# Kernel optimization log

Hardware: AMD Instinct MI355X
Metric: run time of the kernel (lower is better)

## Reference

```python
import jax, jax.numpy as jnp
import numpy as np

EPS = 1e-12
W_MAX = 0.8
ALPHA_MAX = 1.5
T = 10
ETA = 0.2
ALPHA_SCALE = 1.0
N = 50000
IN_DIM = 512
HID = 256
C = 8
EH = 64
E2 = 400000  # undirected pairs; E = 2*E2 directed edges


def setup_inputs() -> dict:
    key = jax.random.key(0)
    ks = jax.random.split(key, 12)
    x = jax.random.normal(ks[0], (N, IN_DIM), jnp.float32)
    src0 = jax.random.randint(ks[1], (E2,), 0, N)
    dst0 = jax.random.randint(ks[2], (E2,), 0, N)
    edge_index = jnp.concatenate([jnp.stack([src0, dst0]), jnp.stack([dst0, src0])], axis=1)
    rev = jnp.concatenate([jnp.arange(E2) + E2, jnp.arange(E2)])
    def lin(k, i, o):
        return jax.random.normal(k, (i, o), jnp.float32) * (2.0 / i) ** 0.5
    enc_w1 = lin(ks[3], IN_DIM, HID); enc_b1 = jnp.zeros((HID,), jnp.float32)
    enc_w2 = lin(ks[4], HID, C); enc_b2 = jnp.zeros((C,), jnp.float32)
    edge_w1 = lin(ks[5], 2 * HID + 2, EH); edge_b1 = jnp.zeros((EH,), jnp.float32)
    edge_w2 = lin(ks[6], EH, 1); edge_b2 = jnp.zeros((1,), jnp.float32)
    bound = (6.0 / (C + C)) ** 0.5  # xavier_uniform
    R_raw = jax.random.uniform(ks[7], (C, C), jnp.float32, -bound, bound) + 0.5 * jnp.eye(C, dtype=jnp.float32)
    R_scale_log = jnp.float32(0.0)
    msg_logit = jnp.float32(-3.0)
    return dict(x=x, edge_index=edge_index, rev=rev,
                enc_w1=enc_w1, enc_b1=enc_b1, enc_w2=enc_w2, enc_b2=enc_b2,
                edge_w1=edge_w1, edge_b1=edge_b1, edge_w2=edge_w2, edge_b2=edge_b2,
                R_raw=R_raw, R_scale_log=R_scale_log, msg_logit=msg_logit)


def reference(x, edge_index, rev, enc_w1, enc_b1, enc_w2, enc_b2,
              edge_w1, edge_b1, edge_w2, edge_b2, R_raw, R_scale_log, msg_logit):
    num_nodes = x.shape[0]
    src, dst = edge_index[0], edge_index[1]
    # unary encoder (mlp type, eval mode -> no dropout)
    h = jax.nn.relu(x @ enc_w1 + enc_b1)
    logits = h @ enc_w2 + enc_b2
    log_phi = jax.nn.log_softmax(logits, axis=-1)  # [N, C]
    # structural edge features from out-degree of src
    deg = jax.ops.segment_sum(jnp.ones_like(src, jnp.float32), src, num_segments=num_nodes)
    logdeg = jnp.log(deg + 1.0)
    a, b = logdeg[src], logdeg[dst]
    struct = jnp.stack([a + b, jnp.abs(a - b)], axis=-1)  # [E, 2]
    # learned symmetric edge weights -> per-edge kernel K
    hs, hd = h[src], h[dst]
    edge_in = jnp.concatenate([hs * hd, jnp.abs(hs - hd), struct], axis=-1)  # [E, 2H+2]
    eh = jax.nn.relu(edge_in @ edge_w1 + edge_b1)
    w_raw = (eh @ edge_w2 + edge_b2)[:, 0]
    w = W_MAX * jax.nn.sigmoid(w_raw)
    w = 0.5 * (w + w[rev])
    R = 0.5 * (R_raw + R_raw.T)
    R = (jax.nn.softplus(R_scale_log) + 1e-06) * jnp.tanh(R)
    K = jnp.exp(w[:, None, None] * R[None])  # [E, C, C]
    degc = jnp.maximum(deg, 1.0)
    edge_norm = (degc[src] * degc[dst]) ** -0.5  # [E]
    alpha = ALPHA_MAX * jax.nn.sigmoid(msg_logit) * ALPHA_SCALE
    lp_src = log_phi[src]
    m = jax.nn.softmax(lp_src, axis=-1)  # init_unary=True

    def step(m, _):
        f = jnp.einsum('ec,ecd->ed', m, K)
        log_f = jnp.log(jnp.maximum(f, EPS)) * edge_norm[:, None]
        sum_in = jax.ops.segment_sum(log_f, dst, num_segments=num_nodes)
        excl = sum_in[src] - log_f[rev]
        m_new = jax.nn.softmax(lp_src + alpha * excl, axis=-1)
        m = (1.0 - ETA) * m + ETA * m_new
        m = jnp.maximum(m, EPS)
        m = m / m.sum(axis=-1, keepdims=True)
        return m, None

    m, _ = jax.lax.scan(step, m, None, length=T)
    # beliefs
    f = jnp.einsum('ec,ecd->ed', m, K)
    log_f = jnp.log(jnp.maximum(f, EPS)) * edge_norm[:, None]
    sum_in = jax.ops.segment_sum(log_f, dst, num_segments=num_nodes)
    beliefs = jax.nn.softmax(log_phi + alpha * sum_in, axis=-1)
    return beliefs
```

## Files before the change

kernel.cpp:

```cpp
#include <hip/hip_runtime.h>
#include <cstddef>
#include <cstdint>

typedef _Float16 h4 __attribute__((ext_vector_type(4)));
typedef _Float16 h8 __attribute__((ext_vector_type(8)));
typedef float    f4 __attribute__((ext_vector_type(4)));
typedef int      i4 __attribute__((ext_vector_type(4)));

#define NN      50000
#define IND     512
#define HIDN    256
#define E2P     400000
#define EDD     800000
#define NBLK    196
#define SCN     50176
#define EBLK    1563
#define DBLK    3125

#define OFF_HF16    ((size_t)0)
#define OFF_LOGF    ((size_t)0)
#define OFF_Z       ((size_t)25600000)
#define OFF_DEG     ((size_t)28800000)
#define OFF_LOGDEG  ((size_t)29004800)
#define OFF_DEGC    ((size_t)29204800)
#define OFF_BASE    ((size_t)29404800)
#define OFF_CNT     ((size_t)29609600)
#define OFF_BLK     ((size_t)29814400)
#define OFF_WT      ((size_t)29818496)
#define OFF_BT      ((size_t)30080640)
#define OFF_RS      ((size_t)30150272)
#define OFF_WSYM    ((size_t)30150784)
#define OFF_POS     ((size_t)31750784)
#define OFF_ORDER   ((size_t)34950784)
#define OFF_BASE2   ((size_t)36550784)
#define OFF_OFS2    ((size_t)36755584)
#define OFF_EIS     ((size_t)36960384)
#define OFF_M2      ((size_t)40160384)
#define OFF_REC     ((size_t)52960384)
#define WS_NEED     ((size_t)65760384)

__device__ __forceinline__ int key2(int s, int d) {
    return ((s >> 10) << 10) | (d >> 6);
}

__device__ __forceinline__ int xcd_swz(int bid, int nwg) {
    int q = nwg >> 3, r = nwg & 7;
    int x = bid & 7, idx = bid >> 3;
    return (x < r ? x * (q + 1) : r * (q + 1) + (x - r) * q) + idx;
}

__global__ void k_deg(const int* __restrict__ ei, int* __restrict__ deg,
                      int* __restrict__ cnt2) {
    int e = blockIdx.x * 256 + threadIdx.x;
    int v = ei[e];
    atomicAdd(&deg[v], 1);
    if (e < E2P) {
        int d = ei[EDD + e];
        atomicAdd(&cnt2[key2(v, d)], 1);
    }
}

__global__ void k_node(const int* __restrict__ deg, float* __restrict__ logdeg,
                       float* __restrict__ degc) {
    int n = blockIdx.x * 256 + threadIdx.x;
    if (n < NN) {
        float d = (float)deg[n];
        logdeg[n] = logf(d + 1.0f);
        degc[n]   = fmaxf(d, 1.0f);
    }
}

__global__ void k_scan1(const int* __restrict__ deg, int* __restrict__ incl,
                        int* __restrict__ blk) {
    __shared__ int sm[256];
    int i = blockIdx.x * 256 + threadIdx.x;
    int v = deg[i];
    sm[threadIdx.x] = v;
    __syncthreads();
    for (int off = 1; off < 256; off <<= 1) {
        int t = (threadIdx.x >= off) ? sm[threadIdx.x - off] : 0;
        __syncthreads();
        sm[threadIdx.x] += t;
        __syncthreads();
    }
    incl[i] = sm[threadIdx.x];
    if (threadIdx.x == 255) blk[blockIdx.x] = sm[255];
}

__global__ void k_scan2(int* __restrict__ blk) {
    __shared__ int sm[256];
    int v = (threadIdx.x < NBLK) ? blk[threadIdx.x] : 0;
    sm[threadIdx.x] = v;
    __syncthreads();
    for (int off = 1; off < 256; off <<= 1) {
        int t = (threadIdx.x >= off) ? sm[threadIdx.x - off] : 0;
        __syncthreads();
        sm[threadIdx.x] += t;
        __syncthreads();
    }
    if (threadIdx.x < NBLK) blk[threadIdx.x] = sm[threadIdx.x];
}

__global__ void k_scan3(const int* __restrict__ incl, const int* __restrict__ deg,
                        const int* __restrict__ blk, int* __restrict__ base) {
    int i = blockIdx.x * 256 + threadIdx.x;
    int off = (blockIdx.x > 0) ? blk[blockIdx.x - 1] : 0;
    base[i] = off + incl[i] - deg[i];
}

__global__ void k_pos(const int* __restrict__ ei, const int* __restrict__ base,
                      int* __restrict__ cnt, int* __restrict__ pos) {
    int e = blockIdx.x * 256 + threadIdx.x;
    int dstn = ei[EDD + e];
    pos[e] = base[dstn] + atomicAdd(&cnt[dstn], 1);
}

__global__ void k_order(const int* __restrict__ ei, const int* __restrict__ base2,
                        int* __restrict__ ofs2, int* __restrict__ order) {
    int p = blockIdx.x * 256 + threadIdx.x;
    if (p < E2P) {
        int k = key2(ei[p], ei[EDD + p]);
        order[base2[k] + atomicAdd(&ofs2[k], 1)] = p;
    }
}

__global__ void k_gath(const int* __restrict__ ei, const int* __restrict__ order,
                       int2* __restrict__ eiS) {
    int i = blockIdx.x * 256 + threadIdx.x;
    if (i < E2P) {
        int p = order[i];
        eiS[i] = make_int2(ei[p], ei[EDD + p]);
    }
}

__global__ void k_prep(const float* __restrict__ enc_w1, const float* __restrict__ edge_w1,
                       const float* __restrict__ R_raw, const float* __restrict__ Rsl,
                       const float* __restrict__ mlog,
                       _Float16* __restrict__ Wt, _Float16* __restrict__ Bt,
                       float* __restrict__ Rs) {
    int gid = blockIdx.x * 256 + threadIdx.x;
    if (gid < 256 * 512) {
        int n = gid >> 9, k = gid & 511;
        Wt[n * 512 + k] = (_Float16)enc_w1[k * 256 + n];
        return;
    }
    int g2 = gid - 256 * 512;
    if (g2 < 64 * 544) {
        int n = g2 / 544, k = g2 - n * 544;
        float v = 0.0f;
        if (k < 512) {
            int tm = k >> 5, r = k & 31;
            int qq = r >> 3, jj = (r >> 1) & 3, typ = k & 1;
            int c = (tm >> 1) * 32 + qq * 8 + (tm & 1) * 4 + jj;
            v = edge_w1[(typ ? 256 + c : c) * 64 + n];
        } else if (k < 514) {
            v = edge_w1[k * 64 + n];
        }
        Bt[n * 544 + k] = (_Float16)v;
        return;
    }
    int g3 = g2 - 64 * 544;
    if (g3 < 64) {
        int c = g3 >> 3, d = g3 & 7;
        float rv = 0.5f * (R_raw[c * 8 + d] + R_raw[d * 8 + c]);
        float s  = log1pf(expf(Rsl[0])) + 1e-6f;
        Rs[g3] = s * tanhf(rv);
        return;
    }
    if (g3 == 64) {
        Rs[64] = 1.5f / (1.0f + expf(-mlog[0]));
    }
}

__global__ __launch_bounds__(256) void k_enc(const float* __restrict__ x,
                                             const _Float16* __restrict__ Wt,
                                             const float* __restrict__ b1,
                                             _Float16* __restrict__ hf) {
    __shared__ _Float16 WL[2][256 * 40];
    const int tid = threadIdx.x;
    const int wid = tid >> 6;
    const int lane = tid & 63;
    const int l15 = lane & 15;
    const int q = lane >> 4;
    const int m0 = blockIdx.x * 64;
    const int row = m0 + wid * 16 + l15;
    const bool ract = (row < NN);
    const float* xrow = x + (size_t)row * IND;

    f4 acc[16];
#pragma unroll
    for (int i = 0; i < 16; i++) acc[i] = (f4){0.f, 0.f, 0.f, 0.f};

    const int wn  = tid >> 2;
    const int wo  = (tid & 3) * 8;

    h8 wreg[4];
#pragma unroll
    for (int rep = 0; rep < 4; rep++)
        wreg[rep] = *(const h8*)(Wt + (size_t)(rep * 64 + wn) * IND + wo);
    f4 xa = (f4){0, 0, 0, 0}, xb = (f4){0, 0, 0, 0};
    if (ract) {
        const f4* xp = (const f4*)(xrow + q * 8);
        xa = xp[0]; xb = xp[1];
    }

    for (int kt = 0; kt < 16; kt++) {
        const int cur = kt & 1;
#pragma unroll
        for (int rep = 0; rep < 4; rep++)
            *(h8*)&WL[cur][(rep * 64 + wn) * 40 + wo] = wreg[rep];
        __syncthreads();
        f4 xa2, xb2;
        if (kt < 15) {
            const int kc = (kt + 1) * 32;
#pragma unroll
            for (int rep = 0; rep < 4; rep++)
                wreg[rep] = *(const h8*)(Wt + (size_t)(rep * 64 + wn) * IND + kc + wo);
            if (ract) {
                const f4* xp = (const f4*)(xrow + kc + q * 8);
                xa2 = xp[0]; xb2 = xp[1];
            }
        }
        h8 a;
#pragma unroll
        for (int u = 0; u < 4; u++) { a[u] = (_Float16)xa[u]; a[4 + u] = (_Float16)xb[u]; }
#pragma unroll
        for (int nt = 0; nt < 16; nt++) {
            h8 b = *(const h8*)&WL[cur][(nt * 16 + l15) * 40 + q * 8];
            acc[nt] = __builtin_amdgcn_mfma_f32_16x16x32_f16(a, b, acc[nt], 0, 0, 0);
        }
        if (kt < 15 && ract) { xa = xa2; xb = xb2; }
        __syncthreads();
    }
#pragma unroll
    for (int nt = 0; nt < 16; nt++) {
        int col = nt * 16 + l15;
        float bv = b1[col];
#pragma unroll
        for (int reg = 0; reg < 4; reg++) {
            int orow = m0 + wid * 16 + q * 4 + reg;
            if (orow < NN) {
                float v = acc[nt][reg] + bv;
                hf[(size_t)orow * HIDN + col] = (_Float16)fmaxf(v, 0.f);
            }
        }
    }
}

__global__ void k_logits(const _Float16* __restrict__ hf, const float* __restrict__ w2,
                         const float* __restrict__ b2, float* __restrict__ Z) {
    __shared__ float w2L[2048];
    for (int i = threadIdx.x; i < 2048; i += 256) w2L[i] = w2[i];
    __syncthreads();
    int n = blockIdx.x * 256 + threadIdx.x;
    if (n >= NN) return;
    float sum[8];
#pragma unroll
    for (int c = 0; c < 8; c++) sum[c] = b2[c];
    for (int kb = 0; kb < 32; kb++) {
        h8 hv = *(const h8*)(hf + (size_t)n * HIDN + kb * 8);
#pragma unroll
        for (int u = 0; u < 8; u++) {
            float hx = (float)hv[u];
            const float* wr = &w2L[(kb * 8 + u) * 8];
#pragma unroll
            for (int c = 0; c < 8; c++) sum[c] += hx * wr[c];
        }
    }
    float mx = sum[0];
#pragma unroll
    for (int c = 1; c < 8; c++) mx = fmaxf(mx, sum[c]);
    float se = 0.f;
#pragma unroll
    for (int c = 0; c < 8; c++) se += __expf(sum[c] - mx);
    float lse = __logf(se);
#pragma unroll
    for (int c = 0; c < 8; c++) Z[(size_t)n * 16 + c] = sum[c] - mx - lse;
}

__global__ __launch_bounds__(256) void k_edge(const int2* __restrict__ eiS,
        const _Float16* __restrict__ hf, const float* __restrict__ logdeg,
        const _Float16* __restrict__ BtG, const float* __restrict__ eb1,
        const float* __restrict__ ew2, const float* __restrict__ eb2,
        float* __restrict__ wsym2) {
    __shared__ _Float16 BtL[64 * 136];
    const int tid = threadIdx.x;
    const int wid = tid >> 6;
    const int lane = tid & 63;
    const int l15 = lane & 15;
    const int q = lane >> 4;
    const int eb = xcd_swz(blockIdx.x, gridDim.x) * 128;

    int sidx[2], didx[2];
    float la[2], lb[2];
#pragma unroll
    for (int mt = 0; mt < 2; mt++) {
        int e = eb + wid * 32 + mt * 16 + l15;
        int2 sd = eiS[e];
        sidx[mt] = sd.x;
        didx[mt] = sd.y;
        la[mt] = logdeg[sidx[mt]];
        lb[mt] = logdeg[didx[mt]];
    }

    f4 acc[2][4];
#pragma unroll
    for (int a = 0; a < 2; a++)
#pragma unroll
        for (int b = 0; b < 4; b++) acc[a][b] = (f4){0.f, 0.f, 0.f, 0.f};

    const _Float16* hq = hf + q * 8;
    h8 curS[2], curD[2];
#pragma unroll
    for (int mt = 0; mt < 2; mt++) {
        curS[mt] = *(const h8*)(hq + (size_t)sidx[mt] * HIDN);
        curD[mt] = *(const h8*)(hq + (size_t)didx[mt] * HIDN);
    }

    for (int ph = 0; ph < 4; ph++) {
        __syncthreads();
        {
            const int r = tid >> 2;
            const int c0 = tid & 3;
            const int kbase = ph * 128;
#pragma unroll
            for (int i2 = 0; i2 < 4; i2++) {
                int ck = c0 + i2 * 4;
                *(h8*)&BtL[r * 136 + ck * 8] =
                    *(const h8*)(BtG + (size_t)r * 544 + kbase + ck * 8);
            }
        }
        __syncthreads();
#pragma unroll
        for (int kk2 = 0; kk2 < 2; kk2++) {
            const int kk = ph * 2 + kk2;
            h8 nxtS[2], nxtD[2];
            if (kk < 7) {
                const int c1 = (kk + 1) * 32;
#pragma unroll
                for (int mt = 0; mt < 2; mt++) {
                    nxtS[mt] = *(const h8*)(hq + (size_t)sidx[mt] * HIDN + c1);
                    nxtD[mt] = *(const h8*)(hq + (size_t)didx[mt] * HIDN + c1);
                }
            }
            const int ko = kk2 * 64 + q * 8;
            {
                h8 a0[2];
#pragma unroll
                for (int mt = 0; mt < 2; mt++) {
#pragma unroll
                    for (int j = 0; j < 4; j++) {
                        float x1 = (float)curS[mt][j], x2 = (float)curD[mt][j];
                        a0[mt][2 * j]     = (_Float16)(x1 * x2);
                        a0[mt][2 * j + 1] = (_Float16)fabsf(x1 - x2);
                    }
                }
                h8 bf[4];
#pragma unroll
                for (int nt = 0; nt < 4; nt++)
                    bf[nt] = *(const h8*)&BtL[(nt * 16 + l15) * 136 + ko];
#pragma unroll
                for (int mt = 0; mt < 2; mt++)
#pragma unroll
                    for (int nt = 0; nt < 4; nt++)
                        acc[mt][nt] = __builtin_amdgcn_mfma_f32_16x16x32_f16(a0[mt], bf[nt], acc[mt][nt], 0, 0, 0);
            }
            {
                h8 a1[2];
#pragma unroll
                for (int mt = 0; mt < 2; mt++) {
#pragma unroll
                    for (int j = 0; j < 4; j++) {
                        float x1 = (float)curS[mt][4 + j], x2 = (float)curD[mt][4 + j];
                        a1[mt][2 * j]     = (_Float16)(x1 * x2);
                        a1[mt][2 * j + 1] = (_Float16)fabsf(x1 - x2);
                    }
                }
                h8 bf[4];
#pragma unroll
                for (int nt = 0; nt < 4; nt++)
                    bf[nt] = *(const h8*)&BtL[(nt * 16 + l15) * 136 + ko + 32];
#pragma unroll
                for (int mt = 0; mt < 2; mt++)
#pragma unroll
                    for (int nt = 0; nt < 4; nt++)
                        acc[mt][nt] = __builtin_amdgcn_mfma_f32_16x16x32_f16(a1[mt], bf[nt], acc[mt][nt], 0, 0, 0);
            }
            if (kk < 7) {
#pragma unroll
                for (int mt = 0; mt < 2; mt++) { curS[mt] = nxtS[mt]; curD[mt] = nxtD[mt]; }
            }
        }
    }

    __syncthreads();
    {
        const int r = tid >> 2, ck = tid & 3;
        *(h8*)&BtL[r * 136 + ck * 8] = *(const h8*)(BtG + (size_t)r * 544 + 512 + ck * 8);
    }
    __syncthreads();
    {
        h8 bf[4];
#pragma unroll
        for (int nt = 0; nt < 4; nt++)
            bf[nt] = *(const h8*)&BtL[(nt * 16 + l15) * 136 + q * 8];
#pragma unroll
        for (int mt = 0; mt < 2; mt++) {
            h8 a = (h8){0, 0, 0, 0, 0, 0, 0, 0};
            if (q == 0) {
                a[0] = (_Float16)(la[mt] + lb[mt]);
                a[1] = (_Float16)fabsf(la[mt] - lb[mt]);
            }
#pragma unroll
            for (int nt = 0; nt < 4; nt++)
                acc[mt][nt] = __builtin_amdgcn_mfma_f32_16x16x32_f16(a, bf[nt], acc[mt][nt], 0, 0, 0);
        }
    }

    float b1v[4], w2v[4];
#pragma unroll
    for (int nt = 0; nt < 4; nt++) {
        int col = nt * 16 + l15;
        b1v[nt] = eb1[col];
        w2v[nt] = ew2[col];
    }
    const float b2s = eb2[0];
    float part[2][4];
#pragma unroll
    for (int mt = 0; mt < 2; mt++)
#pragma unroll
        for (int reg = 0; reg < 4; reg++) {
            float s = 0.f;
#pragma unroll
            for (int nt = 0; nt < 4; nt++) {
                float v = acc[mt][nt][reg] + b1v[nt];
                s += fmaxf(v, 0.f) * w2v[nt];
            }
            part[mt][reg] = s;
        }
#pragma unroll
    for (int off = 1; off < 16; off <<= 1)
#pragma unroll
        for (int mt = 0; mt < 2; mt++)
#pragma unroll
            for (int reg = 0; reg < 4; reg++)
                part[mt][reg] += __shfl_xor(part[mt][reg], off, 64);
    if (l15 == 0) {
#pragma unroll
        for (int mt = 0; mt < 2; mt++)
#pragma unroll
            for (int reg = 0; reg < 4; reg++) {
                int er = eb + wid * 32 + mt * 16 + q * 4 + reg;
                if (er < E2P) {
                    float xr = part[mt][reg] + b2s;
                    wsym2[er] = 0.8f / (1.0f + __expf(-xr));
                }
            }
    }
}


__device__ __forceinline__ void kprod1(const float* __restrict__ RsL, float w,
                                       const float* m, float* f) {
#pragma unroll
    for (int d = 0; d < 8; d++) f[d] = 0.f;
#pragma unroll
    for (int c = 0; c < 8; c++) {
        {
            float kv = __expf(w * RsL[c * 8 + c]);
            f[c] += m[c] * kv;
        }
#pragma unroll
        for (int d = c + 1; d < 8; d++) {
            float kv = __expf(w * RsL[c * 8 + d]);
            f[d] += m[c] * kv;
            f[c] += m[d] * kv;
        }
    }
}

__global__ __launch_bounds__(256) void k_init(const int2* __restrict__ eiS,
        const float* __restrict__ wsym2, const float* __restrict__ degc,
        const float* __restrict__ Rs, const float* __restrict__ Z,
        const int* __restrict__ pos, const int* __restrict__ order,
        i4* __restrict__ rec, _Float16* __restrict__ M2,
        _Float16* __restrict__ logf) {
    __shared__ float RsL[64];
    const int tid = threadIdx.x;
    if (tid < 64) RsL[tid] = Rs[tid];
    __syncthreads();
    int i = xcd_swz(blockIdx.x, EBLK) * 256 + tid;
    if (i >= E2P) return;
    int p = order[i];
    int2 sd = eiS[i];
    int sp = sd.x, dp = sd.y;
    float w = wsym2[i];
    float nrm = rsqrtf(degc[sp] * degc[dp]);
    int pz0 = pos[p], pz1 = pos[E2P + p];
    rec[2 * i]     = (i4){sp, pz0, (int)__float_as_int(w), (int)__float_as_int(nrm)};
    rec[2 * i + 1] = (i4){dp, pz1, (int)__float_as_int(w), (int)__float_as_int(nrm)};
    const f4* Zs = (const f4*)(Z + (size_t)sp * 16);
    const f4* Zd = (const f4*)(Z + (size_t)dp * 16);
    f4 ls0 = Zs[0], ls1 = Zs[1], ld0 = Zd[0], ld1 = Zd[1];
    float lps[8], lpd[8];
#pragma unroll
    for (int u = 0; u < 4; u++) { lps[u] = ls0[u]; lps[4+u] = ls1[u]; lpd[u] = ld0[u]; lpd[4+u] = ld1[u]; }
    float me[8], mr[8];
    {
        float mx = lps[0], mx2 = lpd[0];
#pragma unroll
        for (int d = 1; d < 8; d++) { mx = fmaxf(mx, lps[d]); mx2 = fmaxf(mx2, lpd[d]); }
        float s = 0.f, s2 = 0.f;
#pragma unroll
        for (int d = 0; d < 8; d++) { me[d] = __expf(lps[d] - mx); s += me[d];
                                      mr[d] = __expf(lpd[d] - mx2); s2 += mr[d]; }
        float rs = 1.f / s, rs2 = 1.f / s2;
#pragma unroll
        for (int d = 0; d < 8; d++) { me[d] *= rs; mr[d] *= rs2; }
    }
    {
        h8 mh, mh2;
#pragma unroll
        for (int d = 0; d < 8; d++) { mh[d] = (_Float16)me[d]; mh2[d] = (_Float16)mr[d]; }
        *(h8*)(M2 + (size_t)(2 * i) * 8)     = mh;
        *(h8*)(M2 + (size_t)(2 * i + 1) * 8) = mh2;
    }
    float fe[8], fr[8];
    kprod1(RsL, w, me, fe);
    kprod1(RsL, w, mr, fr);
    h8 le, lr;
#pragma unroll
    for (int d = 0; d < 8; d++) {
        le[d] = (_Float16)(__logf(fmaxf(fe[d], 1e-12f)) * nrm);
        lr[d] = (_Float16)(__logf(fmaxf(fr[d], 1e-12f)) * nrm);
    }
    *(h8*)(logf + (size_t)pz0 * 8) = le;
    *(h8*)(logf + (size_t)pz1 * 8) = lr;
}

__global__ __launch_bounds__(256) void k_bp2(const i4* __restrict__ rec,
        const float* __restrict__ Rs, const float* __restrict__ Z,
        _Float16* __restrict__ M2, _Float16* __restrict__ logf) {
    __shared__ float RsL[64];
    const int tid = threadIdx.x;
    if (tid < 64) RsL[tid] = Rs[tid];
    __syncthreads();
    const int qq = xcd_swz(blockIdx.x, DBLK) * 256 + tid;
    i4 r = rec[qq];
    const int node = r[0], pz = r[1];
    const float w = __int_as_float(r[2]), nrm = __int_as_float(r[3]);
    const float alpha = Rs[64];
    h8 mh = *(const h8*)(M2 + (size_t)qq * 8);
    float m[8];
#pragma unroll
    for (int d = 0; d < 8; d++) m[d] = (float)mh[d];
    float f[8];
    kprod1(RsL, w, m, f);
    float lf[8], lfo[8];
#pragma unroll
    for (int d = 0; d < 8; d++) lf[d] = __logf(fmaxf(f[d], 1e-12f)) * nrm;
#pragma unroll
    for (int d = 0; d < 8; d++) lfo[d] = __shfl_xor(lf[d], 1, 64);
    const f4* Zr = (const f4*)(Z + (size_t)node * 16);
    f4 z0 = Zr[0], z1 = Zr[1], z2 = Zr[2], z3 = Zr[3];
    float t[8];
#pragma unroll
    for (int u = 0; u < 4; u++) {
        t[u]     = z0[u] + alpha * (z2[u] - lfo[u]);
        t[4 + u] = z1[u] + alpha * (z3[u] - lfo[4 + u]);
    }
    float m1[8];
    {
        float mx = t[0];
#pragma unroll
        for (int d = 1; d < 8; d++) mx = fmaxf(mx, t[d]);
        float s = 0.f;
#pragma unroll
        for (int d = 0; d < 8; d++) { m1[d] = __expf(t[d] - mx); s += m1[d]; }
        float rs = 1.f / s;
        float t1 = 0.f;
#pragma unroll
        for (int d = 0; d < 8; d++) {
            m1[d] = fmaxf(0.8f * m[d] + 0.2f * m1[d] * rs, 1e-12f); t1 += m1[d];
        }
        float rt = 1.f / t1;
#pragma unroll
        for (int d = 0; d < 8; d++) m1[d] *= rt;
    }
    {
        h8 mo;
#pragma unroll
        for (int d = 0; d < 8; d++) mo[d] = (_Float16)m1[d];
        *(h8*)(M2 + (size_t)qq * 8) = mo;
    }
    float f2[8];
    kprod1(RsL, w, m1, f2);
    h8 le;
#pragma unroll
    for (int d = 0; d < 8; d++)
        le[d] = (_Float16)(__logf(fmaxf(f2[d], 1e-12f)) * nrm);
    *(h8*)(logf + (size_t)pz * 8) = le;
}

__global__ void k_sum(const _Float16* __restrict__ logf, const int* __restrict__ base,
                      const int* __restrict__ deg, float* __restrict__ Z,
                      const float* __restrict__ Rs, float* __restrict__ out, int fin) {
    int g = blockIdx.x * 256 + threadIdx.x;
    int n = g >> 3;
    if (n >= NN) return;
    int j = threadIdx.x & 7;
    int b = base[n], cnt = deg[n];
    float acc[8];
#pragma unroll
    for (int d = 0; d < 8; d++) acc[d] = 0.f;
    for (int s = j; s < cnt; s += 8) {
        h8 v = *(const h8*)(logf + (size_t)(b + s) * 8);
#pragma unroll
        for (int d = 0; d < 8; d++) acc[d] += (float)v[d];
    }
    int lane = threadIdx.x & 63;
    float v4[4], v2[2], r;
    {
        bool hi = (lane & 4) != 0;
#pragma unroll
        for (int i = 0; i < 4; i++) {
            float send = hi ? acc[i] : acc[i + 4];
            float recv = __shfl_xor(send, 4, 64);
            v4[i] = (hi ? acc[i + 4] : acc[i]) + recv;
        }
    }
    {
        bool hi = (lane & 2) != 0;
#pragma unroll
        for (int i = 0; i < 2; i++) {
            float send = hi ? v4[i] : v4[i + 2];
            float recv = __shfl_xor(send, 2, 64);
            v2[i] = (hi ? v4[i + 2] : v4[i]) + recv;
        }
    }
    {
        bool hi = (lane & 1) != 0;
        float send = hi ? v2[0] : v2[1];
        float recv = __shfl_xor(send, 1, 64);
        r = (hi ? v2[1] : v2[0]) + recv;
    }
    if (!fin) {
        Z[(size_t)n * 16 + 8 + j] = r;
    } else {
        float alpha = Rs[64];
        float v = Z[(size_t)n * 16 + j] + alpha * r;
        float mx = v;
        mx = fmaxf(mx, __shfl_xor(mx, 1, 64));
        mx = fmaxf(mx, __shfl_xor(mx, 2, 64));
        mx = fmaxf(mx, __shfl_xor(mx, 4, 64));
        float ex = __expf(v - mx);
        float s = ex;
        s += __shfl_xor(s, 1, 64); s += __shfl_xor(s, 2, 64); s += __shfl_xor(s, 4, 64);
        out[(size_t)n * 8 + j] = ex / s;
    }
}

extern "C" void kernel_launch(void* const* d_in, const int* in_sizes, int n_in,
                              void* d_out, int out_size, void* d_ws, size_t ws_size,
                              hipStream_t stream) {
    if (ws_size < WS_NEED) return;
    const float* x        = (const float*)d_in[0];
    const int*   ei       = (const int*)d_in[1];
    const float* enc_w1   = (const float*)d_in[3];
    const float* enc_b1   = (const float*)d_in[4];
    const float* enc_w2   = (const float*)d_in[5];
    const float* enc_b2   = (const float*)d_in[6];
    const float* edge_w1  = (const float*)d_in[7];
    const float* edge_b1  = (const float*)d_in[8];
    const float* edge_w2  = (const float*)d_in[9];
    const float* edge_b2  = (const float*)d_in[10];
    const float* R_raw    = (const float*)d_in[11];
    const float* Rsl      = (const float*)d_in[12];
    const float* mlog     = (const float*)d_in[13];

    char* ws = (char*)d_ws;
    _Float16* hf     = (_Float16*)(ws + OFF_HF16);
    _Float16* logfb  = (_Float16*)(ws + OFF_LOGF);
    float* Zb        = (float*)(ws + OFF_Z);
    int*   deg       = (int*)  (ws + OFF_DEG);
    float* logdeg    = (float*)(ws + OFF_LOGDEG);
    float* degc      = (float*)(ws + OFF_DEGC);
    int*   baseA     = (int*)  (ws + OFF_BASE);
    int*   cnt       = (int*)  (ws + OFF_CNT);
    int*   blk       = (int*)  (ws + OFF_BLK);
    _Float16* Wt     = (_Float16*)(ws + OFF_WT);
    _Float16* Bt     = (_Float16*)(ws + OFF_BT);
    float* Rs        = (float*)(ws + OFF_RS);
    float* wsym2     = (float*)(ws + OFF_WSYM);
    int*   pos       = (int*)  (ws + OFF_POS);
    int*   order     = (int*)  (ws + OFF_ORDER);
    int*   base2     = (int*)  (ws + OFF_BASE2);
    int*   ofs2      = (int*)  (ws + OFF_OFS2);
    int2*  eiS       = (int2*) (ws + OFF_EIS);
    _Float16* M2b    = (_Float16*)(ws + OFF_M2);
    i4*    rec       = (i4*)   (ws + OFF_REC);
    float* outp      = (float*)d_out;

    hipMemsetAsync(deg, 0, (size_t)SCN * 4, stream);
    hipMemsetAsync(ofs2, 0, (size_t)SCN * 4, stream);
    k_deg<<<dim3(EDD / 256), dim3(256), 0, stream>>>(ei, deg, ofs2);
    k_node<<<dim3(NBLK), dim3(256), 0, stream>>>(deg, logdeg, degc);
    k_prep<<<dim3((256 * 512 + 64 * 544 + 65 + 255) / 256), dim3(256), 0, stream>>>(
        enc_w1, edge_w1, R_raw, Rsl, mlog, Wt, Bt, Rs);
    k_scan1<<<dim3(NBLK), dim3(256), 0, stream>>>(deg, cnt , blk);
    k_scan2<<<dim3(1), dim3(256), 0, stream>>>(blk);
    k_scan3<<<dim3(NBLK), dim3(256), 0, stream>>>(cnt, deg, blk, baseA);
    hipMemsetAsync(cnt, 0, (size_t)SCN * 4, stream);
    k_pos<<<dim3(EDD / 256), dim3(256), 0, stream>>>(ei, baseA, cnt, pos);
    k_scan1<<<dim3(NBLK), dim3(256), 0, stream>>>(ofs2, cnt, blk);
    k_scan2<<<dim3(1), dim3(256), 0, stream>>>(blk);
    k_scan3<<<dim3(NBLK), dim3(256), 0, stream>>>(cnt, ofs2, blk, base2);
    hipMemsetAsync(ofs2, 0, (size_t)SCN * 4, stream);
    k_order<<<dim3(EBLK), dim3(256), 0, stream>>>(ei, base2, ofs2, order);
    k_gath<<<dim3(EBLK), dim3(256), 0, stream>>>(ei, order, eiS);
    k_enc<<<dim3((NN + 63) / 64), dim3(256), 0, stream>>>(x, Wt, enc_b1, hf);
    k_logits<<<dim3(NBLK), dim3(256), 0, stream>>>(hf, enc_w2, enc_b2, Zb);
    k_edge<<<dim3(E2P / 128), dim3(256), 0, stream>>>(eiS, hf, logdeg, Bt, edge_b1,
                                                      edge_w2, edge_b2, wsym2);
    k_init<<<dim3(EBLK), dim3(256), 0, stream>>>(eiS, wsym2, degc, Rs, Zb, pos, order,
                                                 rec, M2b, logfb);
    k_sum<<<dim3((NN * 8 + 255) / 256), dim3(256), 0, stream>>>(logfb, baseA, deg, Zb,
                                                                Rs, outp, 0);
    for (int t = 0; t < 10; t++) {
        k_bp2<<<dim3(DBLK), dim3(256), 0, stream>>>(rec, Rs, Zb, M2b, logfb);
        k_sum<<<dim3((NN * 8 + 255) / 256), dim3(256), 0, stream>>>(logfb, baseA, deg, Zb,
                                                                    Rs, outp, (t == 9) ? 1 : 0);
    }
    (void)in_sizes; (void)n_in; (void)out_size;
}
```

Baseline: 816.6 us.

## Fuse segment-sum into node-centric BP iteration with ping-pong log_f buffers

Replaces the edge-parallel BP kernel plus separate per-node segment-sum with one node-centric kernel. Each group of 8 lanes sums a node's incoming log messages, then processes that node's outgoing edges, writing new log messages to a second buffer at the reverse-edge slot. Edge data is re-laid out in destination-sorted order (w, norm, partner position), and M is stored per slot. This halves the launches per iteration and removes the Z round-trip for sums, at the cost of scattered writes via ppos, reading each in-edge's log_f twice, and load imbalance across high-degree nodes.

```diff
diff --git a/kernel.cpp b/kernel.cpp
--- a/kernel.cpp
+++ b/kernel.cpp
@@ -15,10 +15,11 @@
 #define NBLK    196
 #define SCN     50176
 #define EBLK    1563
-#define DBLK    3125
+#define NBPN    1563
 
 #define OFF_HF16    ((size_t)0)
-#define OFF_LOGF    ((size_t)0)
+#define OFF_LOGFA   ((size_t)0)
+#define OFF_LOGFB   ((size_t)12800000)
 #define OFF_Z       ((size_t)25600000)
 #define OFF_DEG     ((size_t)28800000)
 #define OFF_LOGDEG  ((size_t)29004800)
@@ -35,9 +36,10 @@
 #define OFF_BASE2   ((size_t)36550784)
 #define OFF_OFS2    ((size_t)36755584)
 #define OFF_EIS     ((size_t)36960384)
-#define OFF_M2      ((size_t)40160384)
-#define OFF_REC     ((size_t)52960384)
-#define WS_NEED     ((size_t)65760384)
+#define OFF_M       ((size_t)40160384)
+#define OFF_WNS     ((size_t)52960384)
+#define OFF_PPOS    ((size_t)59360384)
+#define WS_NEED     ((size_t)62560384)
 
 __device__ __forceinline__ int key2(int s, int d) {
     return ((s >> 10) << 10) | (d >> 6);
@@ -483,8 +485,8 @@
         const float* __restrict__ wsym2, const float* __restrict__ degc,
         const float* __restrict__ Rs, const float* __restrict__ Z,
         const int* __restrict__ pos, const int* __restrict__ order,
-        i4* __restrict__ rec, _Float16* __restrict__ M2,
-        _Float16* __restrict__ logf) {
+        float2* __restrict__ wnS, int* __restrict__ ppos,
+        _Float16* __restrict__ M, _Float16* __restrict__ logfA) {
     __shared__ float RsL[64];
     const int tid = threadIdx.x;
     if (tid < 64) RsL[tid] = Rs[tid];
@@ -496,9 +498,12 @@
     int sp = sd.x, dp = sd.y;
     float w = wsym2[i];
     float nrm = rsqrtf(degc[sp] * degc[dp]);
-    int pz0 = pos[p], pz1 = pos[E2P + p];
-    rec[2 * i]     = (i4){sp, pz0, (int)__float_as_int(w), (int)__float_as_int(nrm)};
-    rec[2 * i + 1] = (i4){dp, pz1, (int)__float_as_int(w), (int)__float_as_int(nrm)};
+    int pz0 = pos[p];
+    int pz1 = pos[E2P + p];
+    wnS[pz0] = make_float2(w, nrm);
+    wnS[pz1] = make_float2(w, nrm);
+    ppos[pz0] = pz1;
+    ppos[pz1] = pz0;
     const f4* Zs = (const f4*)(Z + (size_t)sp * 16);
     const f4* Zd = (const f4*)(Z + (size_t)dp * 16);
     f4 ls0 = Zs[0], ls1 = Zs[1], ld0 = Zd[0], ld1 = Zd[1];
@@ -522,8 +527,8 @@
         h8 mh, mh2;
 #pragma unroll
         for (int d = 0; d < 8; d++) { mh[d] = (_Float16)me[d]; mh2[d] = (_Float16)mr[d]; }
-        *(h8*)(M2 + (size_t)(2 * i) * 8)     = mh;
-        *(h8*)(M2 + (size_t)(2 * i + 1) * 8) = mh2;
+        *(h8*)(M + (size_t)pz1 * 8) = mh;
+        *(h8*)(M + (size_t)pz0 * 8) = mh2;
     }
     float fe[8], fr[8];
     kprod1(RsL, w, me, fe);
@@ -534,77 +539,83 @@
         le[d] = (_Float16)(__logf(fmaxf(fe[d], 1e-12f)) * nrm);
         lr[d] = (_Float16)(__logf(fmaxf(fr[d], 1e-12f)) * nrm);
     }
-    *(h8*)(logf + (size_t)pz0 * 8) = le;
-    *(h8*)(logf + (size_t)pz1 * 8) = lr;
-}
-
-__global__ __launch_bounds__(256) void k_bp2(const i4* __restrict__ rec,
-        const float* __restrict__ Rs, const float* __restrict__ Z,
-        _Float16* __restrict__ M2, _Float16* __restrict__ logf) {
+    *(h8*)(logfA + (size_t)pz0 * 8) = le;
+    *(h8*)(logfA + (size_t)pz1 * 8) = lr;
+}
+
+__global__ __launch_bounds__(256) void k_bpN(const float* __restrict__ Rs,
+        const float* __restrict__ Z, const int* __restrict__ base,
+        const int* __restrict__ deg, const float2* __restrict__ wnS,
+        const int* __restrict__ ppos, _Float16* __restrict__ M,
+        const _Float16* __restrict__ lfA, _Float16* __restrict__ lfB) {
     __shared__ float RsL[64];
     const int tid = threadIdx.x;
     if (tid < 64) RsL[tid] = Rs[tid];
     __syncthreads();
-    const int qq = xcd_swz(blockIdx.x, DBLK) * 256 + tid;
-    i4 r = rec[qq];
-    const int node = r[0], pz = r[1];
-    const float w = __int_as_float(r[2]), nrm = __int_as_float(r[3]);
+    int g = xcd_swz(blockIdx.x, NBPN) * 256 + tid;
+    int n = g >> 3;
+    if (n >= NN) return;
+    const int j = tid & 7;
+    const int b = base[n], cnt = deg[n];
     const float alpha = Rs[64];
-    h8 mh = *(const h8*)(M2 + (size_t)qq * 8);
-    float m[8];
-#pragma unroll
-    for (int d = 0; d < 8; d++) m[d] = (float)mh[d];
-    float f[8];
-    kprod1(RsL, w, m, f);
-    float lf[8], lfo[8];
-#pragma unroll
-    for (int d = 0; d < 8; d++) lf[d] = __logf(fmaxf(f[d], 1e-12f)) * nrm;
-#pragma unroll
-    for (int d = 0; d < 8; d++) lfo[d] = __shfl_xor(lf[d], 1, 64);
-    const f4* Zr = (const f4*)(Z + (size_t)node * 16);
-    f4 z0 = Zr[0], z1 = Zr[1], z2 = Zr[2], z3 = Zr[3];
-    float t[8];
-#pragma unroll
-    for (int u = 0; u < 4; u++) {
-        t[u]     = z0[u] + alpha * (z2[u] - lfo[u]);
-        t[4 + u] = z1[u] + alpha * (z3[u] - lfo[4 + u]);
-    }
-    float m1[8];
-    {
+    const f4* Zr = (const f4*)(Z + (size_t)n * 16);
+    f4 z0 = Zr[0], z1 = Zr[1];
+    float lp[8];
+#pragma unroll
+    for (int u = 0; u < 4; u++) { lp[u] = z0[u]; lp[4 + u] = z1[u]; }
+    float S[8];
+#pragma unroll
+    for (int d = 0; d < 8; d++) S[d] = 0.f;
+    for (int s = j; s < cnt; s += 8) {
+        h8 v = *(const h8*)(lfA + (size_t)(b + s) * 8);
+#pragma unroll
+        for (int d = 0; d < 8; d++) S[d] += (float)v[d];
+    }
+#pragma unroll
+    for (int off = 1; off < 8; off <<= 1)
+#pragma unroll
+        for (int d = 0; d < 8; d++) S[d] += __shfl_xor(S[d], off, 64);
+    for (int s = j; s < cnt; s += 8) {
+        const int sl = b + s;
+        h8 lfh = *(const h8*)(lfA + (size_t)sl * 8);
+        h8 mh  = *(const h8*)(M + (size_t)sl * 8);
+        float2 wn = wnS[sl];
+        float t[8], m1[8];
+#pragma unroll
+        for (int d = 0; d < 8; d++)
+            t[d] = lp[d] + alpha * (S[d] - (float)lfh[d]);
         float mx = t[0];
 #pragma unroll
         for (int d = 1; d < 8; d++) mx = fmaxf(mx, t[d]);
-        float s = 0.f;
-#pragma unroll
-        for (int d = 0; d < 8; d++) { m1[d] = __expf(t[d] - mx); s += m1[d]; }
-        float rs = 1.f / s;
-        float t1 = 0.f;
+        float ssum = 0.f;
+#pragma unroll
+        for (int d = 0; d < 8; d++) { m1[d] = __expf(t[d] - mx); ssum += m1[d]; }
+        float rs = 1.f / ssum, t1 = 0.f;
 #pragma unroll
         for (int d = 0; d < 8; d++) {
-            m1[d] = fmaxf(0.8f * m[d] + 0.2f * m1[d] * rs, 1e-12f); t1 += m1[d];
+            m1[d] = fmaxf(0.8f * (float)mh[d] + 0.2f * m1[d] * rs, 1e-12f);
+            t1 += m1[d];
         }
         float rt = 1.f / t1;
 #pragma unroll
         for (int d = 0; d < 8; d++) m1[d] *= rt;
-    }
-    {
         h8 mo;
 #pragma unroll
         for (int d = 0; d < 8; d++) mo[d] = (_Float16)m1[d];
-        *(h8*)(M2 + (size_t)qq * 8) = mo;
-    }
-    float f2[8];
-    kprod1(RsL, w, m1, f2);
-    h8 le;
-#pragma unroll
-    for (int d = 0; d < 8; d++)
-        le[d] = (_Float16)(__logf(fmaxf(f2[d], 1e-12f)) * nrm);
-    *(h8*)(logf + (size_t)pz * 8) = le;
+        *(h8*)(M + (size_t)sl * 8) = mo;
+        float f2[8];
+        kprod1(RsL, wn.x, m1, f2);
+        h8 le;
+#pragma unroll
+        for (int d = 0; d < 8; d++)
+            le[d] = (_Float16)(__logf(fmaxf(f2[d], 1e-12f)) * wn.y);
+        *(h8*)(lfB + (size_t)ppos[sl] * 8) = le;
+    }
 }
 
 __global__ void k_sum(const _Float16* __restrict__ logf, const int* __restrict__ base,
-                      const int* __restrict__ deg, float* __restrict__ Z,
-                      const float* __restrict__ Rs, float* __restrict__ out, int fin) {
+                      const int* __restrict__ deg, const float* __restrict__ Z,
+                      const float* __restrict__ Rs, float* __restrict__ out) {
     int g = blockIdx.x * 256 + threadIdx.x;
     int n = g >> 3;
     if (n >= NN) return;
@@ -644,20 +655,16 @@
         float recv = __shfl_xor(send, 1, 64);
         r = (hi ? v2[1] : v2[0]) + recv;
     }
-    if (!fin) {
-        Z[(size_t)n * 16 + 8 + j] = r;
-    } else {
-        float alpha = Rs[64];
-        float v = Z[(size_t)n * 16 + j] + alpha * r;
-        float mx = v;
-        mx = fmaxf(mx, __shfl_xor(mx, 1, 64));
-        mx = fmaxf(mx, __shfl_xor(mx, 2, 64));
-        mx = fmaxf(mx, __shfl_xor(mx, 4, 64));
-        float ex = __expf(v - mx);
-        float s = ex;
-        s += __shfl_xor(s, 1, 64); s += __shfl_xor(s, 2, 64); s += __shfl_xor(s, 4, 64);
-        out[(size_t)n * 8 + j] = ex / s;
-    }
+    float alpha = Rs[64];
+    float v = Z[(size_t)n * 16 + j] + alpha * r;
+    float mx = v;
+    mx = fmaxf(mx, __shfl_xor(mx, 1, 64));
+    mx = fmaxf(mx, __shfl_xor(mx, 2, 64));
+    mx = fmaxf(mx, __shfl_xor(mx, 4, 64));
+    float ex = __expf(v - mx);
+    float s = ex;
+    s += __shfl_xor(s, 1, 64); s += __shfl_xor(s, 2, 64); s += __shfl_xor(s, 4, 64);
+    out[(size_t)n * 8 + j] = ex / s;
 }
 
 extern "C" void kernel_launch(void* const* d_in, const int* in_sizes, int n_in,
@@ -680,7 +687,8 @@
 
     char* ws = (char*)d_ws;
     _Float16* hf     = (_Float16*)(ws + OFF_HF16);
-    _Float16* logfb  = (_Float16*)(ws + OFF_LOGF);
+    _Float16* lfA    = (_Float16*)(ws + OFF_LOGFA);
+    _Float16* lfB    = (_Float16*)(ws + OFF_LOGFB);
     float* Zb        = (float*)(ws + OFF_Z);
     int*   deg       = (int*)  (ws + OFF_DEG);
     float* logdeg    = (float*)(ws + OFF_LOGDEG);
@@ -697,8 +705,9 @@
     int*   base2     = (int*)  (ws + OFF_BASE2);
     int*   ofs2      = (int*)  (ws + OFF_OFS2);
     int2*  eiS       = (int2*) (ws + OFF_EIS);
-    _Float16* M2b    = (_Float16*)(ws + OFF_M2);
-    i4*    rec       = (i4*)   (ws + OFF_REC);
+    _Float16* Mb     = (_Float16*)(ws + OFF_M);
+    float2* wnS      = (float2*)(ws + OFF_WNS);
+    int*   ppos      = (int*)  (ws + OFF_PPOS);
     float* outp      = (float*)d_out;
 
     hipMemsetAsync(deg, 0, (size_t)SCN * 4, stream);
@@ -723,13 +732,15 @@
     k_edge<<<dim3(E2P / 128), dim3(256), 0, stream>>>(eiS, hf, logdeg, Bt, edge_b1,
                                                       edge_w2, edge_b2, wsym2);
     k_init<<<dim3(EBLK), dim3(256), 0, stream>>>(eiS, wsym2, degc, Rs, Zb, pos, order,
-                                                 rec, M2b, logfb);
-    k_sum<<<dim3((NN * 8 + 255) / 256), dim3(256), 0, stream>>>(logfb, baseA, deg, Zb,
-                                                                Rs, outp, 0);
+                                                 wnS, ppos, Mb, lfA);
+    _Float16* cur = lfA;
+    _Float16* nxt = lfB;
     for (int t = 0; t < 10; t++) {
-        k_bp2<<<dim3(DBLK), dim3(256), 0, stream>>>(rec, Rs, Zb, M2b, logfb);
-        k_sum<<<dim3((NN * 8 + 255) / 256), dim3(256), 0, stream>>>(logfb, baseA, deg, Zb,
-                                                                    Rs, outp, (t == 9) ? 1 : 0);
-    }
+        k_bpN<<<dim3(NBPN), dim3(256), 0, stream>>>(Rs, Zb, baseA, deg, wnS, ppos,
+                                                    Mb, cur, nxt);
+        _Float16* tmp = cur; cur = nxt; nxt = tmp;
+    }
+    k_sum<<<dim3((NN * 8 + 255) / 256), dim3(256), 0, stream>>>(cur, baseA, deg, Zb,
+                                                                Rs, outp);
     (void)in_sizes; (void)n_in; (void)out_size;
 }
```

Result: no change. 805.0 us (-1.4%).
